# Performance work log

Hardware: AMD Instinct MI355X
Metric: run time of the kernel (lower is better)

Reference implementation:

```python
import jax, jax.numpy as jnp
import numpy as np

N = 4096
IN_F = 128
OUT_F = 128
H = 4
D = OUT_F // H  # head_out = 32
SLOPE = 0.2
LN_EPS = 1e-5


def setup_inputs() -> dict:
    key = jax.random.key(0)
    k_x, k_adj, k_W, k_a = jax.random.split(key, 4)
    x = jax.random.normal(k_x, (N, IN_F), dtype=jnp.float32)
    adjacency = jax.random.randint(k_adj, (N, N), 0, 2).astype(jnp.bool_)
    # xavier-uniform-ish init scales
    w_std = float(np.sqrt(2.0 / (IN_F + H * D)))
    a_std = float(np.sqrt(2.0 / (H + 2 * D)))
    W = jax.random.normal(k_W, (H * D, IN_F), dtype=jnp.float32) * w_std  # torch Linear weight layout
    a = jax.random.normal(k_a, (H, 2 * D), dtype=jnp.float32) * a_std
    ln_gamma = jnp.ones((OUT_F,), dtype=jnp.float32)
    ln_beta = jnp.zeros((OUT_F,), dtype=jnp.float32)
    return {"x": x, "adjacency": adjacency, "W": W, "a": a,
            "ln_gamma": ln_gamma, "ln_beta": ln_beta}


def reference(x, adjacency, W, a, ln_gamma, ln_beta):
    # Wx: (N, H, D)
    Wx = (x @ W.T).reshape(N, H, D)
    # e[i,j,h] = leaky_relu( <Wx[i,h], a[h,:D]> + <Wx[j,h], a[h,D:]> )
    # (exact factorization of the original cat([Wx_i, Wx_j]) * a sum)
    alpha_i = jnp.einsum('nhd,hd->nh', Wx, a[:, :D])  # source/i term
    alpha_j = jnp.einsum('nhd,hd->nh', Wx, a[:, D:])  # neighbor/j term
    e = alpha_i[:, None, :] + alpha_j[None, :, :]      # (N, N, H)
    e = jnp.where(e >= 0, e, SLOPE * e)                # LeakyReLU
    e = jnp.where(adjacency[:, :, None], e, -jnp.inf)  # mask non-edges
    attn = jax.nn.softmax(e, axis=1)                   # softmax over j
    out = jnp.einsum('ijh,jhd->ihd', attn, Wx).reshape(N, H * D)
    y = out + x                                        # residual (dims match)
    mu = jnp.mean(y, axis=-1, keepdims=True)
    var = jnp.mean((y - mu) ** 2, axis=-1, keepdims=True)
    return ln_gamma * (y - mu) / jnp.sqrt(var + LN_EPS) + ln_beta
```

## Files before the change

### kernel.cpp

```cpp
#include <hip/hip_runtime.h>
#include <stdint.h>

#define NN 4096
#define LOG2E 1.44269504088896340736f

typedef float f32x4 __attribute__((ext_vector_type(4)));
typedef short s16x8 __attribute__((ext_vector_type(8)));
typedef unsigned u32x4 __attribute__((ext_vector_type(4)));
typedef _Float16 f16x2 __attribute__((ext_vector_type(2)));

static __device__ __forceinline__ unsigned f32_to_bf16_rne(float f) {
    unsigned u = __builtin_bit_cast(unsigned, f);
    return (u + 0x7FFFu + ((u >> 16) & 1u)) >> 16;
}
static __device__ __forceinline__ unsigned f16bits(float f) {
    _Float16 h = (_Float16)f;
    return (unsigned)__builtin_bit_cast(unsigned short, h);
}

__global__ __launch_bounds__(256) void k01(const unsigned* __restrict__ adj_raw,
                                           const float* __restrict__ x,
                                           const float* __restrict__ W,
                                           const float* __restrict__ a,
                                           unsigned* __restrict__ bits,
                                           unsigned* __restrict__ wxb16,
                                           float* __restrict__ ai_s,
                                           unsigned* __restrict__ ejfj) {
    const int t = threadIdx.x;
    if (blockIdx.x < 2048) {
        __shared__ int s_i32;
        if (t == 0) {
            int all_small = 1;
            for (int i = 0; i < 32; ++i) all_small &= (adj_raw[i] <= 1u);
            s_i32 = all_small;
        }
        __syncthreads();
        const long o = (long)blockIdx.x * 256 + t;
        unsigned mm = 0;
        if (s_i32) {
            const u32x4* p = (const u32x4*)adj_raw + o * 8;
            #pragma unroll
            for (int g = 0; g < 8; ++g) {
                u32x4 v = p[g];
                mm |= (v.x & 1u) << (g * 4) | (v.y & 1u) << (g * 4 + 1) |
                      (v.z & 1u) << (g * 4 + 2) | (v.w & 1u) << (g * 4 + 3);
            }
        } else {
            const u32x4* p = (const u32x4*)adj_raw + o * 2;
            #pragma unroll
            for (int g = 0; g < 2; ++g) {
                u32x4 v = p[g];
                unsigned d[4] = {v.x, v.y, v.z, v.w};
                #pragma unroll
                for (int qq = 0; qq < 4; ++qq)
                    #pragma unroll
                    for (int b = 0; b < 4; ++b)
                        mm |= ((d[qq] >> (8 * b)) & 1u) << (g * 16 + qq * 4 + b);
            }
        }
        bits[o] = mm;
        return;
    }

    __shared__ unsigned short WL[128 * 136];
    __shared__ unsigned short XL[16 * 136];
    __shared__ float WxF[16 * 132];

    const int bid = blockIdx.x - 2048;
    const int i0 = bid * 16;

    for (int p4 = t; p4 < 4096; p4 += 256) {
        f32x4 w4 = *(const f32x4*)(W + 4 * p4);
        unsigned lo = f32_to_bf16_rne(w4.x) | (f32_to_bf16_rne(w4.y) << 16);
        unsigned hi = f32_to_bf16_rne(w4.z) | (f32_to_bf16_rne(w4.w) << 16);
        int c = (4 * p4) >> 7, k = (4 * p4) & 127;
        *(unsigned long long*)&WL[c * 136 + k] =
            (unsigned long long)lo | ((unsigned long long)hi << 32);
    }
    for (int p4 = t; p4 < 512; p4 += 256) {
        f32x4 x4 = *(const f32x4*)(x + (long)i0 * 128 + 4 * p4);
        unsigned lo = f32_to_bf16_rne(x4.x) | (f32_to_bf16_rne(x4.y) << 16);
        unsigned hi = f32_to_bf16_rne(x4.z) | (f32_to_bf16_rne(x4.w) << 16);
        int r = (4 * p4) >> 7, k = (4 * p4) & 127;
        *(unsigned long long*)&XL[r * 136 + k] =
            (unsigned long long)lo | ((unsigned long long)hi << 32);
    }
    __syncthreads();

    const int w = t >> 6, l = t & 63, m = l & 15, q = l >> 4;
    f32x4 acc0 = {0.f, 0.f, 0.f, 0.f}, acc1 = {0.f, 0.f, 0.f, 0.f};
    #pragma unroll
    for (int ks = 0; ks < 4; ++ks) {
        s16x8 af = *(const s16x8*)&XL[m * 136 + ks * 32 + q * 8];
        s16x8 b0 = *(const s16x8*)&WL[(w * 32 + m) * 136 + ks * 32 + q * 8];
        s16x8 b1 = *(const s16x8*)&WL[(w * 32 + 16 + m) * 136 + ks * 32 + q * 8];
        acc0 = __builtin_amdgcn_mfma_f32_16x16x32_bf16(af, b0, acc0, 0, 0, 0);
        acc1 = __builtin_amdgcn_mfma_f32_16x16x32_bf16(af, b1, acc1, 0, 0, 0);
    }
    const int jblk = i0 >> 5;
    const int qslot = ((i0 & 16) + q * 4) >> 3;
    const int dhalf = q & 1;
    #pragma unroll
    for (int j2 = 0; j2 < 2; ++j2) {
        const int fblk = 2 * w + j2;
        f32x4 acc = j2 ? acc1 : acc0;
        unsigned d01 = f16bits(acc[0]) | (f16bits(acc[1]) << 16);
        unsigned d23 = f16bits(acc[2]) | (f16bits(acc[3]) << 16);
        unsigned* wp = wxb16 + (((jblk * 8 + fblk) * 64 + qslot * 16 + m) << 2) + dhalf * 2;
        wp[0] = d01;
        wp[1] = d23;
        #pragma unroll
        for (int reg = 0; reg < 4; ++reg)
            WxF[(q * 4 + reg) * 132 + fblk * 16 + m] = acc[reg];
    }
    __syncthreads();
    if (t < 64) {
        int r = t >> 2, h = t & 3;
        float s_i = 0.f, s_j = 0.f;
        const float* ar = a + h * 64;
        #pragma unroll
        for (int d = 0; d < 32; ++d) {
            float wv = WxF[r * 132 + h * 32 + d];
            s_i += wv * ar[d];
            s_j += wv * ar[32 + d];
        }
        ai_s[(i0 + r) * 4 + h] = s_i * LOG2E;
        float sjl = s_j * LOG2E;
        ejfj[h * NN + i0 + r] = f16bits(exp2f(sjl)) | (f16bits(exp2f(0.2f * sjl)) << 16);
    }
}

__global__ __launch_bounds__(1024, 4) void k2_attn(
        const float* __restrict__ x,
        const unsigned* __restrict__ adjbits,
        const unsigned* __restrict__ wxb16,
        const float* __restrict__ ai_s,
        const unsigned* __restrict__ ejfj,
        const float* __restrict__ gamma,
        const float* __restrict__ beta,
        float* __restrict__ out) {
    __shared__ unsigned efL[4][4096];
    __shared__ unsigned maskL[16][132];
    __shared__ float C_lds[4][16][32];
    __shared__ float l_lds[4][16];

    const int t = threadIdx.x;
    const int i0 = blockIdx.x * 16;
    const int w = t >> 6, l = t & 63;
    const int h = w & 3, p = w >> 2;
    const int m = l & 15, q = l >> 4;

    {
        const u32x4* src = (const u32x4*)ejfj;
        u32x4* dst = (u32x4*)&efL[0][0];
        #pragma unroll
        for (int g = 0; g < 4; ++g) dst[t + 1024 * g] = src[t + 1024 * g];
    }
    {
        #pragma unroll
        for (int g = 0; g < 2; ++g) {
            int idx = t + 1024 * g;
            int r = idx >> 7, c = idx & 127;
            maskL[r][c] = adjbits[(long)(i0 + r) * 128 + c];
        }
    }
    const float aif = ai_s[(i0 + m) * 4 + h];
    const _Float16 eiH = (_Float16)exp2f(aif);
    const _Float16 fiH = (_Float16)exp2f(0.2f * aif);
    const f16x2 Ei2 = {eiH, eiH};
    const f16x2 Fi2 = {fiH, fiH};
    __syncthreads();

    const unsigned* bp16 = wxb16 + ((2 * h) * 64 + l) * 4;
    const unsigned* efh = &efL[h][0] + q * 8;
    const s16x8 ONESH = {0x3C00, 0x3C00, 0x3C00, 0x3C00,
                         0x3C00, 0x3C00, 0x3C00, 0x3C00};

    f32x4 acc0 = {0.f, 0.f, 0.f, 0.f}, acc1 = {0.f, 0.f, 0.f, 0.f};
    f32x4 accl = {0.f, 0.f, 0.f, 0.f};

    const int ks1 = (p + 4 < 128) ? p + 4 : p;
    u32x4 pa0 = *(const u32x4*)(bp16 + p * 2048);
    u32x4 pb0 = *(const u32x4*)(bp16 + p * 2048 + 256);
    u32x4 pa1 = *(const u32x4*)(bp16 + ks1 * 2048);
    u32x4 pb1 = *(const u32x4*)(bp16 + ks1 * 2048 + 256);

    for (int ks = p; ks < 128; ks += 4) {
        const int ksn2 = (ks + 8 < 128) ? (ks + 8) : ks;
        u32x4 pa2 = *(const u32x4*)(bp16 + ksn2 * 2048);
        u32x4 pb2 = *(const u32x4*)(bp16 + ksn2 * 2048 + 256);

        unsigned mq = (maskL[m][ks] >> (q * 8)) & 0xffu;
        u32x4 ef0 = *(const u32x4*)(efh + ks * 32);
        u32x4 ef1 = *(const u32x4*)(efh + ks * 32 + 4);
        unsigned efu[8] = {ef0.x, ef0.y, ef0.z, ef0.w, ef1.x, ef1.y, ef1.z, ef1.w};

        union { s16x8 v; unsigned u[4]; } af;
        #pragma unroll
        for (int pr = 0; pr < 4; ++pr) {
            unsigned d0 = efu[2 * pr], d1 = efu[2 * pr + 1];
            unsigned Ep = __builtin_amdgcn_perm(d1, d0, 0x05040100);
            unsigned Fp = __builtin_amdgcn_perm(d1, d0, 0x07060302);
            f16x2 mE = Ei2 * __builtin_bit_cast(f16x2, Ep);
            f16x2 mF = Fi2 * __builtin_bit_cast(f16x2, Fp);
            f16x2 mx = __builtin_elementwise_max(mE, mF);
            unsigned lo = (unsigned)(-(int)((mq >> (2 * pr)) & 1u));
            unsigned hi = (unsigned)(-(int)((mq >> (2 * pr + 1)) & 1u));
            unsigned msk = (lo & 0xFFFFu) | (hi & 0xFFFF0000u);
            af.u[pr] = __builtin_bit_cast(unsigned, mx) & msk;
        }
        union { u32x4 u; s16x8 s; } b0c, b1c;
        b0c.u = pa0; b1c.u = pb0;
        acc0 = __builtin_amdgcn_mfma_f32_16x16x32_f16(af.v, b0c.s, acc0, 0, 0, 0);
        acc1 = __builtin_amdgcn_mfma_f32_16x16x32_f16(af.v, b1c.s, acc1, 0, 0, 0);
        accl = __builtin_amdgcn_mfma_f32_16x16x32_f16(af.v, ONESH, accl, 0, 0, 0);
        pa0 = pa1; pb0 = pb1; pa1 = pa2; pb1 = pb2;
    }

    if (p == 0) {
        #pragma unroll
        for (int reg = 0; reg < 4; ++reg) {
            C_lds[h][q * 4 + reg][m] = acc0[reg];
            C_lds[h][q * 4 + reg][16 + m] = acc1[reg];
            if (m == 0) l_lds[h][q * 4 + reg] = accl[reg];
        }
    }
    __syncthreads();
    if (p == 1) {
        #pragma unroll
        for (int reg = 0; reg < 4; ++reg) {
            C_lds[h][q * 4 + reg][m] += acc0[reg];
            C_lds[h][q * 4 + reg][16 + m] += acc1[reg];
            if (m == 0) l_lds[h][q * 4 + reg] += accl[reg];
        }
    }
    __syncthreads();
    if (p == 2) {
        #pragma unroll
        for (int reg = 0; reg < 4; ++reg) {
            C_lds[h][q * 4 + reg][m] += acc0[reg];
            C_lds[h][q * 4 + reg][16 + m] += acc1[reg];
            if (m == 0) l_lds[h][q * 4 + reg] += accl[reg];
        }
    }
    __syncthreads();
    if (p == 3) {
        #pragma unroll
        for (int reg = 0; reg < 4; ++reg) {
            C_lds[h][q * 4 + reg][m] += acc0[reg];
            C_lds[h][q * 4 + reg][16 + m] += acc1[reg];
            if (m == 0) l_lds[h][q * 4 + reg] += accl[reg];
        }
    }
    __syncthreads();

    if (t < 512) {
        const int r = t >> 5, c32 = t & 31;
        const int f0 = c32 * 4;
        const int hh = f0 >> 5, cl = f0 & 31;
        const float linv = 1.0f / l_lds[hh][r];
        f32x4 xv = *(const f32x4*)(x + (long)(i0 + r) * 128 + f0);
        float y[4], s1 = 0.f, s2 = 0.f;
        #pragma unroll
        for (int kk = 0; kk < 4; ++kk) {
            float yy = C_lds[hh][r][cl + kk] * linv + xv[kk];
            y[kk] = yy; s1 += yy; s2 += yy * yy;
        }
        #pragma unroll
        for (int s = 1; s <= 16; s <<= 1) {
            s1 += __shfl_xor(s1, s, 64);
            s2 += __shfl_xor(s2, s, 64);
        }
        const float mean = s1 * (1.0f / 128.0f);
        const float var = s2 * (1.0f / 128.0f) - mean * mean;
        const float rstd = rsqrtf(var + 1e-5f);
        f32x4 gv = *(const f32x4*)(gamma + f0);
        f32x4 bv = *(const f32x4*)(beta + f0);
        f32x4 ov;
        #pragma unroll
        for (int kk = 0; kk < 4; ++kk)
            ov[kk] = gv[kk] * ((y[kk] - mean) * rstd) + bv[kk];
        *(f32x4*)(out + (long)(i0 + r) * 128 + f0) = ov;
    }
}

extern "C" void kernel_launch(void* const* d_in, const int* in_sizes, int n_in,
                              void* d_out, int out_size, void* d_ws, size_t ws_size,
                              hipStream_t stream) {
    const float* x = (const float*)d_in[0];
    const unsigned* adj_raw = (const unsigned*)d_in[1];
    const float* W = (const float*)d_in[2];
    const float* a = (const float*)d_in[3];
    const float* gamma = (const float*)d_in[4];
    const float* beta = (const float*)d_in[5];

    unsigned* wxb16 = (unsigned*)d_ws;
    float* ai_s = (float*)((char*)d_ws + (1 << 20));
    unsigned* ejfj = (unsigned*)((char*)d_ws + (1 << 20) + (64 << 10));
    unsigned* adjbits = (unsigned*)((char*)d_ws + (2 << 20));

    k01<<<2304, 256, 0, stream>>>(adj_raw, x, W, a, adjbits, wxb16, ai_s, ejfj);
    k2_attn<<<256, 1024, 0, stream>>>(x, adjbits, wxb16, ai_s, ejfj, gamma, beta,
                                      (float*)d_out);
}
```

Measured before the change: 129.4 us.

## Split attention over two j-halves and reduce with a separate LayerNorm kernel

The attention kernel now splits the neighbor dimension into two halves per 16-row tile, doubling the grid from 256 to 512 blocks so it fills more of the GPU's compute units. Each block writes its unnormalized partial accumulator and softmax denominator to workspace. A new third kernel sums the two partials, normalizes, adds the residual and applies LayerNorm. This adds an extra launch and a global round trip for the partial results in exchange for more parallelism and a smaller LDS footprint per block.

```diff
diff --git a/kernel.cpp b/kernel.cpp
--- a/kernel.cpp
+++ b/kernel.cpp
@@ -131,38 +131,37 @@
 }
 
 __global__ __launch_bounds__(1024, 4) void k2_attn(
-        const float* __restrict__ x,
         const unsigned* __restrict__ adjbits,
         const unsigned* __restrict__ wxb16,
         const float* __restrict__ ai_s,
         const unsigned* __restrict__ ejfj,
-        const float* __restrict__ gamma,
-        const float* __restrict__ beta,
-        float* __restrict__ out) {
-    __shared__ unsigned efL[4][4096];
-    __shared__ unsigned maskL[16][132];
+        float* __restrict__ Cbuf,
+        float* __restrict__ lbuf) {
+    __shared__ unsigned efL[4][2048];
+    __shared__ unsigned maskL[16][68];
     __shared__ float C_lds[4][16][32];
     __shared__ float l_lds[4][16];
 
     const int t = threadIdx.x;
-    const int i0 = blockIdx.x * 16;
+    const int i0 = (blockIdx.x >> 1) * 16;
+    const int jh = blockIdx.x & 1;
+    const int ksb = jh * 64;
     const int w = t >> 6, l = t & 63;
     const int h = w & 3, p = w >> 2;
     const int m = l & 15, q = l >> 4;
 
     {
-        const u32x4* src = (const u32x4*)ejfj;
-        u32x4* dst = (u32x4*)&efL[0][0];
-        #pragma unroll
-        for (int g = 0; g < 4; ++g) dst[t + 1024 * g] = src[t + 1024 * g];
+        #pragma unroll
+        for (int g = 0; g < 2; ++g) {
+            int v = t + 1024 * g;
+            int head = v >> 9, off = v & 511;
+            ((u32x4*)&efL[head][0])[off] =
+                ((const u32x4*)(ejfj + head * NN + jh * 2048))[off];
+        }
     }
     {
-        #pragma unroll
-        for (int g = 0; g < 2; ++g) {
-            int idx = t + 1024 * g;
-            int r = idx >> 7, c = idx & 127;
-            maskL[r][c] = adjbits[(long)(i0 + r) * 128 + c];
-        }
+        int r = t >> 6, c = t & 63;
+        maskL[r][c] = adjbits[(long)(i0 + r) * 128 + ksb + c];
     }
     const float aif = ai_s[(i0 + m) * 4 + h];
     const _Float16 eiH = (_Float16)exp2f(aif);
@@ -179,20 +178,22 @@
     f32x4 acc0 = {0.f, 0.f, 0.f, 0.f}, acc1 = {0.f, 0.f, 0.f, 0.f};
     f32x4 accl = {0.f, 0.f, 0.f, 0.f};
 
-    const int ks1 = (p + 4 < 128) ? p + 4 : p;
-    u32x4 pa0 = *(const u32x4*)(bp16 + p * 2048);
-    u32x4 pb0 = *(const u32x4*)(bp16 + p * 2048 + 256);
+    const int ks0 = ksb + p;
+    const int ks1 = (p + 4 < 64) ? ks0 + 4 : ks0;
+    u32x4 pa0 = *(const u32x4*)(bp16 + ks0 * 2048);
+    u32x4 pb0 = *(const u32x4*)(bp16 + ks0 * 2048 + 256);
     u32x4 pa1 = *(const u32x4*)(bp16 + ks1 * 2048);
     u32x4 pb1 = *(const u32x4*)(bp16 + ks1 * 2048 + 256);
 
-    for (int ks = p; ks < 128; ks += 4) {
-        const int ksn2 = (ks + 8 < 128) ? (ks + 8) : ks;
+    for (int ks = ks0; ks < ksb + 64; ks += 4) {
+        const int ksn2 = (ks + 8 < ksb + 64) ? (ks + 8) : ks;
         u32x4 pa2 = *(const u32x4*)(bp16 + ksn2 * 2048);
         u32x4 pb2 = *(const u32x4*)(bp16 + ksn2 * 2048 + 256);
 
-        unsigned mq = (maskL[m][ks] >> (q * 8)) & 0xffu;
-        u32x4 ef0 = *(const u32x4*)(efh + ks * 32);
-        u32x4 ef1 = *(const u32x4*)(efh + ks * 32 + 4);
+        const int kl = ks - ksb;
+        unsigned mq = (maskL[m][kl] >> (q * 8)) & 0xffu;
+        u32x4 ef0 = *(const u32x4*)(efh + kl * 32);
+        u32x4 ef1 = *(const u32x4*)(efh + kl * 32 + 4);
         unsigned efu[8] = {ef0.x, ef0.y, ef0.z, ef0.w, ef1.x, ef1.y, ef1.z, ef1.w};
 
         union { s16x8 v; unsigned u[4]; } af;
@@ -258,30 +259,56 @@
         const int r = t >> 5, c32 = t & 31;
         const int f0 = c32 * 4;
         const int hh = f0 >> 5, cl = f0 & 31;
-        const float linv = 1.0f / l_lds[hh][r];
-        f32x4 xv = *(const f32x4*)(x + (long)(i0 + r) * 128 + f0);
-        float y[4], s1 = 0.f, s2 = 0.f;
-        #pragma unroll
-        for (int kk = 0; kk < 4; ++kk) {
-            float yy = C_lds[hh][r][cl + kk] * linv + xv[kk];
-            y[kk] = yy; s1 += yy; s2 += yy * yy;
-        }
-        #pragma unroll
-        for (int s = 1; s <= 16; s <<= 1) {
-            s1 += __shfl_xor(s1, s, 64);
-            s2 += __shfl_xor(s2, s, 64);
-        }
-        const float mean = s1 * (1.0f / 128.0f);
-        const float var = s2 * (1.0f / 128.0f) - mean * mean;
-        const float rstd = rsqrtf(var + 1e-5f);
-        f32x4 gv = *(const f32x4*)(gamma + f0);
-        f32x4 bv = *(const f32x4*)(beta + f0);
-        f32x4 ov;
-        #pragma unroll
-        for (int kk = 0; kk < 4; ++kk)
-            ov[kk] = gv[kk] * ((y[kk] - mean) * rstd) + bv[kk];
-        *(f32x4*)(out + (long)(i0 + r) * 128 + f0) = ov;
-    }
+        f32x4 cv;
+        #pragma unroll
+        for (int kk = 0; kk < 4; ++kk) cv[kk] = C_lds[hh][r][cl + kk];
+        *(f32x4*)(Cbuf + (long)jh * NN * 128 + (long)(i0 + r) * 128 + f0) = cv;
+    }
+    if (t < 64) {
+        int r = t >> 2, hh = t & 3;
+        lbuf[(long)jh * NN * 4 + (i0 + r) * 4 + hh] = l_lds[hh][r];
+    }
+}
+
+__global__ __launch_bounds__(512) void k3_ln(const float* __restrict__ x,
+                                             const float* __restrict__ Cbuf,
+                                             const float* __restrict__ lbuf,
+                                             const float* __restrict__ gamma,
+                                             const float* __restrict__ beta,
+                                             float* __restrict__ out) {
+    const int t = threadIdx.x;
+    const int i0 = blockIdx.x * 16;
+    const int r = t >> 5, c32 = t & 31;
+    const int f0 = c32 * 4;
+    const int hh = f0 >> 5;
+    const long row = i0 + r;
+
+    f32x4 c0 = *(const f32x4*)(Cbuf + row * 128 + f0);
+    f32x4 c1 = *(const f32x4*)(Cbuf + (long)NN * 128 + row * 128 + f0);
+    const float lsum = lbuf[row * 4 + hh] + lbuf[(long)NN * 4 + row * 4 + hh];
+    const float linv = 1.0f / lsum;
+    f32x4 xv = *(const f32x4*)(x + row * 128 + f0);
+    float y[4], s1 = 0.f, s2 = 0.f;
+    #pragma unroll
+    for (int kk = 0; kk < 4; ++kk) {
+        float yy = (c0[kk] + c1[kk]) * linv + xv[kk];
+        y[kk] = yy; s1 += yy; s2 += yy * yy;
+    }
+    #pragma unroll
+    for (int s = 1; s <= 16; s <<= 1) {
+        s1 += __shfl_xor(s1, s, 64);
+        s2 += __shfl_xor(s2, s, 64);
+    }
+    const float mean = s1 * (1.0f / 128.0f);
+    const float var = s2 * (1.0f / 128.0f) - mean * mean;
+    const float rstd = rsqrtf(var + 1e-5f);
+    f32x4 gv = *(const f32x4*)(gamma + f0);
+    f32x4 bv = *(const f32x4*)(beta + f0);
+    f32x4 ov;
+    #pragma unroll
+    for (int kk = 0; kk < 4; ++kk)
+        ov[kk] = gv[kk] * ((y[kk] - mean) * rstd) + bv[kk];
+    *(f32x4*)(out + row * 128 + f0) = ov;
 }
 
 extern "C" void kernel_launch(void* const* d_in, const int* in_sizes, int n_in,
@@ -298,8 +325,10 @@
     float* ai_s = (float*)((char*)d_ws + (1 << 20));
     unsigned* ejfj = (unsigned*)((char*)d_ws + (1 << 20) + (64 << 10));
     unsigned* adjbits = (unsigned*)((char*)d_ws + (2 << 20));
+    float* Cbuf = (float*)((char*)d_ws + (4 << 20));
+    float* lbuf = (float*)((char*)d_ws + (8 << 20));
 
     k01<<<2304, 256, 0, stream>>>(adj_raw, x, W, a, adjbits, wxb16, ai_s, ejfj);
-    k2_attn<<<256, 1024, 0, stream>>>(x, adjbits, wxb16, ai_s, ejfj, gamma, beta,
-                                      (float*)d_out);
-}
+    k2_attn<<<512, 1024, 0, stream>>>(adjbits, wxb16, ai_s, ejfj, Cbuf, lbuf);
+    k3_ln<<<256, 512, 0, stream>>>(x, Cbuf, lbuf, gamma, beta, (float*)d_out);
+}
```

New measurement: 130.0 us. About the same (+0.4%).
